# Kernel tuning notes

Hardware: AMD Instinct MI355X
Metric: run time of the kernel (lower is better)

Reference implementation:

```python
import jax, jax.numpy as jnp
import numpy as np

N = 100_000   # nodes
E = 1_600_000 # edges (COO, directed as given)
D = 128       # input feature dim
H = 128       # hidden dim
L = 3         # layers


def setup_inputs() -> dict:
    key = jax.random.key(0)
    ks = jax.random.split(key, 2 + 2 * L)
    x = jax.random.normal(ks[0], (N, D), dtype=jnp.float32)
    edge_index = jax.random.randint(ks[1], (2, E), 0, N, dtype=jnp.int32)
    inp = {"x": x, "edge_index": edge_index}
    dims = [(D, H), (H, H), (H, H)]
    for i, (fi, fo) in enumerate(dims):
        scale = 1.0 / np.sqrt(fi)
        inp[f"W{i}"] = jax.random.uniform(ks[2 + 2 * i], (fi, fo), jnp.float32, -scale, scale)
        inp[f"b{i}"] = jax.random.uniform(ks[3 + 2 * i], (fo,), jnp.float32, -scale, scale)
    return inp


def reference(x, edge_index, W0, b0, W1, b1, W2, b2):
    n = x.shape[0]
    src, dst = edge_index[0], edge_index[1]
    # GCNConv default: add self-loops, symmetric D^{-1/2}(A+I)D^{-1/2} normalization
    loop = jnp.arange(n, dtype=edge_index.dtype)
    src = jnp.concatenate([src, loop])
    dst = jnp.concatenate([dst, loop])
    ones = jnp.ones(src.shape[0], dtype=x.dtype)
    deg = jax.ops.segment_sum(ones, dst, num_segments=n)          # [N]
    dinv = jnp.where(deg > 0, jax.lax.rsqrt(deg), 0.0)            # deg^{-1/2}, inf->0
    norm = dinv[src] * dinv[dst]                                  # [E+N]

    def gcn_conv(h, W, b):
        h = h @ W                                  # linear transform first (PyG order)
        msg = h[src] * norm[:, None]               # gather + scale, [E+N, H]
        return jax.ops.segment_sum(msg, dst, num_segments=n) + b

    for W, b in ((W0, b0), (W1, b1), (W2, b2)):
        x = jax.nn.relu(gcn_conv(x, W, b))
    return x
```

## Files before the change

### kernel.cpp

```cpp
#include <hip/hip_runtime.h>
#include <hip/hip_bf16.h>

#define TPB 256

typedef short s8v __attribute__((ext_vector_type(8)));
typedef float f4v __attribute__((ext_vector_type(4)));
typedef _Float16 h8v __attribute__((ext_vector_type(8)));

#define PB 128
#define BSHIFT 10
#define BSPAN 1024
#define PCHUNK 4096

__device__ __forceinline__ unsigned short bf16_rne(float v) {
    unsigned int u = __float_as_uint(v);
    u += 0x7fffu + ((u >> 16) & 1u);
    return (unsigned short)(u >> 16);
}
__device__ __forceinline__ void split_bf16(float v, unsigned short& hi, unsigned short& lo) {
    hi = bf16_rne(v);
    float hf = __uint_as_float((unsigned int)hi << 16);
    lo = bf16_rne(v - hf);
}


__global__ __launch_bounds__(256) void bhist_kernel(const int* __restrict__ dst, int E,
                                                    int* __restrict__ bsize) {
    __shared__ int h[PB];
    int t = threadIdx.x;
    if (t < PB) h[t] = 0;
    __syncthreads();
    for (int e = blockIdx.x * 256 + t; e < E; e += gridDim.x * 256)
        atomicAdd(&h[dst[e] >> BSHIFT], 1);
    __syncthreads();
    if (t < PB && h[t] > 0) atomicAdd(&bsize[t], h[t]);
}

__global__ void bscan_kernel(const int* __restrict__ bsize, int* __restrict__ bbase,
                             int* __restrict__ bcursor, int* __restrict__ row, int n, int E) {
    __shared__ int wtot[2];
    int t = threadIdx.x;
    int sz = bsize[t];
    int lane = t & 63, wid = t >> 6;
    int v = sz;
    for (int off = 1; off < 64; off <<= 1) {
        int u = __shfl_up(v, off);
        if (lane >= off) v += u;
    }
    if (lane == 63) wtot[wid] = v;
    __syncthreads();
    if (wid == 1) v += wtot[0];
    bbase[t + 1] = v;
    bcursor[t] = v - sz;
    if (t == 0) { bbase[0] = 0; row[n] = E; }
}

__global__ __launch_bounds__(256) void partition_kernel(const int* __restrict__ src,
                                                        const int* __restrict__ dst, int E,
                                                        int* __restrict__ bcursor,
                                                        int2* __restrict__ part) {
    __shared__ int h[PB];
    __shared__ int gofs[PB];
    int t = threadIdx.x;
    long base = (long)blockIdx.x * PCHUNK;
    int cnt = (int)min((long)PCHUNK, (long)E - base);

    if (t < PB) h[t] = 0;
    __syncthreads();
    for (int j = t; j < cnt; j += 256)
        atomicAdd(&h[dst[base + j] >> BSHIFT], 1);
    __syncthreads();
    if (t < PB) gofs[t] = (h[t] > 0) ? atomicAdd(&bcursor[t], h[t]) : 0;
    __syncthreads();
    if (t < PB) h[t] = 0;
    __syncthreads();
    for (int j = t; j < cnt; j += 256) {
        int s = src[base + j], d = dst[base + j];
        int b = d >> BSHIFT;
        int idx = atomicAdd(&h[b], 1);
        part[(long)gofs[b] + idx] = make_int2(s, d);
    }
}

__global__ __launch_bounds__(1024) void csr_kernel(const int2* __restrict__ part,
                                                   const int* __restrict__ bbase,
                                                   int* __restrict__ row, float* __restrict__ dinv,
                                                   int* __restrict__ esrc, int n) {
    __shared__ int deg[BSPAN];
    __shared__ int lrow[BSPAN];
    __shared__ int cur[BSPAN];
    __shared__ int wsum[16];
    int b = blockIdx.x;
    int n0 = b << BSHIFT;
    int nn = min(BSPAN, n - n0);
    if (nn <= 0) return;
    int e0 = bbase[b], e1 = bbase[b + 1];
    int t = threadIdx.x;

    deg[t] = 0;
    __syncthreads();
    for (int e = e0 + t; e < e1; e += 1024)
        atomicAdd(&deg[part[e].y - n0], 1);
    __syncthreads();

    int a = deg[t];
    int lane = t & 63, wid = t >> 6;
    int v = a;
    for (int off = 1; off < 64; off <<= 1) {
        int u = __shfl_up(v, off);
        if (lane >= off) v += u;
    }
    if (lane == 63) wsum[wid] = v;
    __syncthreads();
    if (wid == 0 && lane < 16) {
        int w = wsum[lane];
        for (int off = 1; off < 16; off <<= 1) {
            int u = __shfl_up(w, off);
            if (lane >= off) w += u;
        }
        wsum[lane] = w;
    }
    __syncthreads();
    int excl = v - a + ((wid > 0) ? wsum[wid - 1] : 0);
    lrow[t] = excl;
    cur[t] = 0;
    if (t < nn) {
        row[n0 + t] = e0 + excl;
        dinv[n0 + t] = rsqrtf((float)(deg[t] + 1));
    }
    __syncthreads();

    for (int e = e0 + t; e < e1; e += 1024) {
        int2 p = part[e];
        int d = p.y - n0;
        int idx = atomicAdd(&cur[d], 1);
        esrc[e0 + lrow[d] + idx] = p.x;
    }
}


__global__ void wsplit_kernel(const float* __restrict__ W0, const float* __restrict__ W1,
                              const float* __restrict__ W2,
                              unsigned short* __restrict__ Whi, unsigned short* __restrict__ Wlo) {
    int t = blockIdx.x * TPB + threadIdx.x;
    if (t >= 3 * 16384) return;
    int layer = t >> 14;
    int e = t & 16383;
    int k = e >> 7, ncol = e & 127;
    const float* W = (layer == 0) ? W0 : (layer == 1) ? W1 : W2;
    unsigned short hi, lo;
    split_bf16(W[e], hi, lo);
    int ct = ncol >> 4;
    int lane = (((k >> 3) & 3) << 4) | (ncol & 15);
    int kki = k >> 5;
    int j = k & 7;
    int idx = layer * 16384 + (((ct * 4 + kki) * 64 + lane) * 8 + j);
    Whi[idx] = hi; Wlo[idx] = lo;
}


__global__ __launch_bounds__(256, 2) void gemm0_mfma(const float* __restrict__ Xf,
                                                     const unsigned short* __restrict__ Whs,
                                                     const unsigned short* __restrict__ Wls,
                                                     _Float16* __restrict__ Ch, int n) {
    __shared__ _Float16 Oh[128 * 128];
    int t = threadIdx.x;
    int wave = t >> 6, lane = t & 63;
    int ch = wave & 1, rh = wave >> 1;
    int lm = lane & 15, q = lane >> 4;
    long row0 = (long)blockIdx.x * 128 + rh * 64;

    const s8v* Wh8 = (const s8v*)Whs;
    const s8v* Wl8 = (const s8v*)Wls;
    s8v Bh[4][4], Bl[4][4];
#pragma unroll
    for (int ct = 0; ct < 4; ct++)
#pragma unroll
        for (int kki = 0; kki < 4; kki++) {
            int idx = (((ch * 4 + ct) * 4 + kki) * 64) + lane;
            Bh[ct][kki] = Wh8[idx];
            Bl[ct][kki] = Wl8[idx];
        }

    f4v acc[4][4];
#pragma unroll
    for (int rt = 0; rt < 4; rt++)
#pragma unroll
        for (int ct = 0; ct < 4; ct++) acc[rt][ct] = (f4v)0.0f;

#pragma unroll
    for (int kki = 0; kki < 4; kki++) {
        s8v ah[4], al[4];
#pragma unroll
        for (int rt = 0; rt < 4; rt++) {
            long r = row0 + rt * 16 + lm;
            long rr = (r < n) ? r : (n - 1);
            const float4* xf4 = (const float4*)(Xf + rr * 128 + kki * 32 + q * 8);
            float4 u0 = xf4[0], u1 = xf4[1];
            float uf[8] = {u0.x, u0.y, u0.z, u0.w, u1.x, u1.y, u1.z, u1.w};
            s8v hv, lv;
#pragma unroll
            for (int j = 0; j < 8; j++) {
                unsigned short hh, ll;
                split_bf16(uf[j], hh, ll);
                hv[j] = (short)hh; lv[j] = (short)ll;
            }
            ah[rt] = hv; al[rt] = lv;
        }
#pragma unroll
        for (int rt = 0; rt < 4; rt++)
#pragma unroll
            for (int ct = 0; ct < 4; ct++) {
                acc[rt][ct] = __builtin_amdgcn_mfma_f32_16x16x32_bf16(ah[rt], Bh[ct][kki], acc[rt][ct], 0, 0, 0);
                acc[rt][ct] = __builtin_amdgcn_mfma_f32_16x16x32_bf16(ah[rt], Bl[ct][kki], acc[rt][ct], 0, 0, 0);
                acc[rt][ct] = __builtin_amdgcn_mfma_f32_16x16x32_bf16(al[rt], Bh[ct][kki], acc[rt][ct], 0, 0, 0);
            }
    }

#pragma unroll
    for (int rt = 0; rt < 4; rt++)
#pragma unroll
        for (int reg = 0; reg < 4; reg++) {
            int lr = rh * 64 + rt * 16 + q * 4 + reg;
#pragma unroll
            for (int ct = 0; ct < 4; ct++)
                Oh[lr * 128 + ch * 64 + ct * 16 + lm] = (_Float16)acc[rt][ct][reg];
        }
    __syncthreads();

    long rowb = (long)blockIdx.x * 128;
    int lr = t >> 1;
    int cb = (t & 1) * 64;
    if (rowb + lr < n) {
        const uint4* s = (const uint4*)&Oh[lr * 128 + cb];
        uint4* d = (uint4*)&Ch[(rowb + lr) * 128 + cb];
#pragma unroll
        for (int u = 0; u < 8; u++) d[u] = s[u];
    }
}


__global__ __launch_bounds__(256) void fused_kernel(const h8v* __restrict__ hIn,
                                                    const float* __restrict__ dinv,
                                                    const int* __restrict__ row,
                                                    const int* __restrict__ esrc,
                                                    const float* __restrict__ bias,
                                                    const unsigned short* __restrict__ Whs,
                                                    const unsigned short* __restrict__ Wls,
                                                    _Float16* __restrict__ hOut, int n) {
    __shared__ float As[16 * 132];
    int t = threadIdx.x;
    int g = t >> 4, lane = t & 15;
    long i = (long)blockIdx.x * 16 + g;

    float r[8];
    if (i < n) {
        float di = dinv[i];
        float s2 = di * di;
        h8v self = hIn[i * 16 + lane];
        float acc[8];
#pragma unroll
        for (int k = 0; k < 8; k++) acc[k] = (float)self[k] * s2;

        int e0 = row[i], e1 = row[i + 1];
        int e = e0;
        for (; e + 4 <= e1; e += 4) {
            int s0 = esrc[e + 0];
            int s1 = esrc[e + 1];
            int s2i = esrc[e + 2];
            int s3 = esrc[e + 3];
            h8v v0 = hIn[(size_t)s0 * 16 + lane];
            h8v v1 = hIn[(size_t)s1 * 16 + lane];
            h8v v2 = hIn[(size_t)s2i * 16 + lane];
            h8v v3 = hIn[(size_t)s3 * 16 + lane];
            float w0 = dinv[s0] * di;
            float w1 = dinv[s1] * di;
            float w2 = dinv[s2i] * di;
            float w3 = dinv[s3] * di;
#pragma unroll
            for (int k = 0; k < 8; k++)
                acc[k] += w0 * (float)v0[k] + w1 * (float)v1[k] + w2 * (float)v2[k] + w3 * (float)v3[k];
        }
        for (; e < e1; ++e) {
            int s = esrc[e];
            h8v v = hIn[(size_t)s * 16 + lane];
            float w = dinv[s] * di;
#pragma unroll
            for (int k = 0; k < 8; k++) acc[k] += w * (float)v[k];
        }

        const float4* b4 = (const float4*)(bias + lane * 8);
        float4 bA = b4[0], bB = b4[1];
        r[0] = fmaxf(acc[0] + bA.x, 0.f); r[1] = fmaxf(acc[1] + bA.y, 0.f);
        r[2] = fmaxf(acc[2] + bA.z, 0.f); r[3] = fmaxf(acc[3] + bA.w, 0.f);
        r[4] = fmaxf(acc[4] + bB.x, 0.f); r[5] = fmaxf(acc[5] + bB.y, 0.f);
        r[6] = fmaxf(acc[6] + bB.z, 0.f); r[7] = fmaxf(acc[7] + bB.w, 0.f);
    } else {
#pragma unroll
        for (int k = 0; k < 8; k++) r[k] = 0.f;
    }

    float* dstA = &As[g * 132 + lane * 8];
    *(float4*)dstA = make_float4(r[0], r[1], r[2], r[3]);
    *(float4*)(dstA + 4) = make_float4(r[4], r[5], r[6], r[7]);
    __syncthreads();

    int w = t >> 6, l64 = t & 63;
    int lm = l64 & 15, q = l64 >> 4;

    const s8v* Wh8 = (const s8v*)Whs;
    const s8v* Wl8 = (const s8v*)Wls;
    s8v Bh[2][4], Bl[2][4];
#pragma unroll
    for (int c = 0; c < 2; c++)
#pragma unroll
        for (int kki = 0; kki < 4; kki++) {
            int idx = (((w * 2 + c) * 4 + kki) * 64) + l64;
            Bh[c][kki] = Wh8[idx];
            Bl[c][kki] = Wl8[idx];
        }

    f4v acc2[2];
    acc2[0] = (f4v)0.0f; acc2[1] = (f4v)0.0f;

#pragma unroll
    for (int kki = 0; kki < 4; kki++) {
        const float* ap = &As[lm * 132 + kki * 32 + q * 8];
        float4 u0 = *(const float4*)ap;
        float4 u1 = *(const float4*)(ap + 4);
        float uf[8] = {u0.x, u0.y, u0.z, u0.w, u1.x, u1.y, u1.z, u1.w};
        s8v hv, lv;
#pragma unroll
        for (int j = 0; j < 8; j++) {
            unsigned short hh, ll;
            split_bf16(uf[j], hh, ll);
            hv[j] = (short)hh; lv[j] = (short)ll;
        }
#pragma unroll
        for (int c = 0; c < 2; c++) {
            acc2[c] = __builtin_amdgcn_mfma_f32_16x16x32_bf16(hv, Bh[c][kki], acc2[c], 0, 0, 0);
            acc2[c] = __builtin_amdgcn_mfma_f32_16x16x32_bf16(hv, Bl[c][kki], acc2[c], 0, 0, 0);
            acc2[c] = __builtin_amdgcn_mfma_f32_16x16x32_bf16(lv, Bh[c][kki], acc2[c], 0, 0, 0);
        }
    }
    __syncthreads();

    _Float16* Oh = (_Float16*)As;
#pragma unroll
    for (int c = 0; c < 2; c++)
#pragma unroll
        for (int reg = 0; reg < 4; reg++)
            Oh[(q * 4 + reg) * 128 + (w * 2 + c) * 16 + lm] = (_Float16)acc2[c][reg];
    __syncthreads();

    long gi = (long)blockIdx.x * 16 + (t >> 4);
    if (gi < n) {
        uint4 v = *(const uint4*)&Oh[t * 8];
        *(uint4*)&hOut[gi * 128 + (size_t)(t & 15) * 8] = v;
    }
}


__global__ __launch_bounds__(256) void agg_final(const h8v* __restrict__ hH,
                                                 const float* __restrict__ dinv,
                                                 const int* __restrict__ row,
                                                 const int* __restrict__ esrc,
                                                 const float* __restrict__ bias,
                                                 float* __restrict__ out, int n) {
    int g    = threadIdx.x >> 4;
    int lane = threadIdx.x & 15;
    int i = blockIdx.x * 16 + g;
    if (i >= n) return;

    float di = dinv[i];
    float s2 = di * di;

    h8v self = hH[(size_t)i * 16 + lane];
    float acc[8];
#pragma unroll
    for (int k = 0; k < 8; k++) acc[k] = (float)self[k] * s2;

    int e0 = row[i], e1 = row[i + 1];
    int e = e0;
    for (; e + 4 <= e1; e += 4) {
        int s0 = esrc[e + 0];
        int s1 = esrc[e + 1];
        int s2i = esrc[e + 2];
        int s3 = esrc[e + 3];
        h8v v0 = hH[(size_t)s0 * 16 + lane];
        h8v v1 = hH[(size_t)s1 * 16 + lane];
        h8v v2 = hH[(size_t)s2i * 16 + lane];
        h8v v3 = hH[(size_t)s3 * 16 + lane];
        float w0 = dinv[s0] * di;
        float w1 = dinv[s1] * di;
        float w2 = dinv[s2i] * di;
        float w3 = dinv[s3] * di;
#pragma unroll
        for (int k = 0; k < 8; k++)
            acc[k] += w0 * (float)v0[k] + w1 * (float)v1[k] + w2 * (float)v2[k] + w3 * (float)v3[k];
    }
    for (; e < e1; ++e) {
        int s = esrc[e];
        h8v v = hH[(size_t)s * 16 + lane];
        float w = dinv[s] * di;
#pragma unroll
        for (int k = 0; k < 8; k++) acc[k] += w * (float)v[k];
    }

    const float4* b4 = (const float4*)(bias + lane * 8);
    float4 bA = b4[0], bB = b4[1];
    float4* o4 = (float4*)(out + (size_t)i * 128 + lane * 8);
    o4[0] = make_float4(fmaxf(acc[0] + bA.x, 0.f), fmaxf(acc[1] + bA.y, 0.f),
                        fmaxf(acc[2] + bA.z, 0.f), fmaxf(acc[3] + bA.w, 0.f));
    o4[1] = make_float4(fmaxf(acc[4] + bB.x, 0.f), fmaxf(acc[5] + bB.y, 0.f),
                        fmaxf(acc[6] + bB.z, 0.f), fmaxf(acc[7] + bB.w, 0.f));
}


extern "C" void kernel_launch(void* const* d_in, const int* in_sizes, int n_in,
                              void* d_out, int out_size, void* d_ws, size_t ws_size,
                              hipStream_t stream) {
    const float* x  = (const float*)d_in[0];
    const int*   ei = (const int*)d_in[1];
    const float* W0 = (const float*)d_in[2];
    const float* b0 = (const float*)d_in[3];
    const float* W1 = (const float*)d_in[4];
    const float* b1 = (const float*)d_in[5];
    const float* W2 = (const float*)d_in[6];
    const float* b2 = (const float*)d_in[7];

    const int H = 128;
    int n = in_sizes[0] / H;
    int E = in_sizes[1] / 2;
    const int* srcp = ei;
    const int* dstp = ei + E;

    int gemm_blocks = (n + 127) / 128;
    long npad = (long)gemm_blocks * 128;
    int nbuck = (n + BSPAN - 1) >> BSHIFT;

    char* p = (char*)d_ws;
    auto alloc = [&](size_t bytes) {
        void* r = (void*)p;
        p += (bytes + 255) & ~(size_t)255;
        return r;
    };
    _Float16* bufH0 = (_Float16*)alloc((size_t)npad * H * 2);
    _Float16* bufH1 = (_Float16*)alloc((size_t)npad * H * 2);
    unsigned short* Whs = (unsigned short*)alloc(3 * 16384 * 2);
    unsigned short* Wls = (unsigned short*)alloc(3 * 16384 * 2);
    float* dinv  = (float*)alloc((size_t)n * sizeof(float));
    int*  row    = (int*)alloc((size_t)(n + 1) * sizeof(int));
    int*  bsize  = (int*)alloc(PB * sizeof(int));
    int*  bbase  = (int*)alloc((PB + 1) * sizeof(int));
    int*  bcursor= (int*)alloc(PB * sizeof(int));
    int2* part   = (int2*)alloc((size_t)E * sizeof(int2));
    int*  esrc   = (int*)alloc((size_t)E * sizeof(int));

    hipMemsetAsync(bsize, 0, PB * sizeof(int), stream);

    bhist_kernel<<<1024, 256, 0, stream>>>(dstp, E, bsize);
    bscan_kernel<<<1, PB, 0, stream>>>(bsize, bbase, bcursor, row, n, E);
    partition_kernel<<<(E + PCHUNK - 1) / PCHUNK, 256, 0, stream>>>(srcp, dstp, E, bcursor, part);
    csr_kernel<<<nbuck, 1024, 0, stream>>>(part, bbase, row, dinv, esrc, n);

    wsplit_kernel<<<(3 * 16384 + TPB - 1) / TPB, TPB, 0, stream>>>(W0, W1, W2, Whs, Wls);

    float* out = (float*)d_out;
    int node_blocks = (n + 15) / 16;

    gemm0_mfma<<<gemm_blocks, 256, 0, stream>>>(x, Whs, Wls, bufH0, n);
    fused_kernel<<<node_blocks, 256, 0, stream>>>((const h8v*)bufH0, dinv, row, esrc, b0,
                                                  Whs + 16384, Wls + 16384, bufH1, n);
    fused_kernel<<<node_blocks, 256, 0, stream>>>((const h8v*)bufH1, dinv, row, esrc, b1,
                                                  Whs + 32768, Wls + 32768, bufH0, n);
    agg_final<<<node_blocks, 256, 0, stream>>>((const h8v*)bufH0, dinv, row, esrc, b2, out, n);
}
```

Before: 409.5 us.

## Fuse weight split into histogram kernel, pad LDS tiles, lower gemm0 register use

The weight bf16 hi/lo split now runs in extra blocks of the edge-histogram kernel, which removes one kernel launch. gemm0 loads its B fragments once per k-step instead of holding all of them in registers, and its launch bound asks for 3 blocks per CU to raise occupancy. The LDS output staging tiles in gemm0 and the fused kernel use a row stride of 136 halfs to reduce bank conflicts. The trade-off is that gemm0 reloads its weight fragments from global memory on every k-step and its LDS footprint grows slightly.

```diff
diff --git a/kernel.cpp b/kernel.cpp
--- a/kernel.cpp
+++ b/kernel.cpp
@@ -11,6 +11,7 @@
 #define BSHIFT 10
 #define BSPAN 1024
 #define PCHUNK 4096
+#define WBLK 192
 
 __device__ __forceinline__ unsigned short bf16_rne(float v) {
     unsigned int u = __float_as_uint(v);
@@ -24,13 +25,38 @@
 }
 
 
-__global__ __launch_bounds__(256) void bhist_kernel(const int* __restrict__ dst, int E,
-                                                    int* __restrict__ bsize) {
+__global__ __launch_bounds__(256) void bhist_wsplit_kernel(const int* __restrict__ dst, int E,
+                                                           int* __restrict__ bsize,
+                                                           const float* __restrict__ W0,
+                                                           const float* __restrict__ W1,
+                                                           const float* __restrict__ W2,
+                                                           unsigned short* __restrict__ Whi,
+                                                           unsigned short* __restrict__ Wlo) {
     __shared__ int h[PB];
     int t = threadIdx.x;
+    if (blockIdx.x < WBLK) {
+        int idx0 = blockIdx.x * 256 + t;
+        if (idx0 < 3 * 16384) {
+            int layer = idx0 >> 14;
+            int e = idx0 & 16383;
+            int k = e >> 7, ncol = e & 127;
+            const float* W = (layer == 0) ? W0 : (layer == 1) ? W1 : W2;
+            unsigned short hi, lo;
+            split_bf16(W[e], hi, lo);
+            int ct = ncol >> 4;
+            int lane = (((k >> 3) & 3) << 4) | (ncol & 15);
+            int kki = k >> 5;
+            int j = k & 7;
+            int oidx = layer * 16384 + (((ct * 4 + kki) * 64 + lane) * 8 + j);
+            Whi[oidx] = hi; Wlo[oidx] = lo;
+        }
+        return;
+    }
+    int blk = blockIdx.x - WBLK;
+    int nblk = gridDim.x - WBLK;
     if (t < PB) h[t] = 0;
     __syncthreads();
-    for (int e = blockIdx.x * 256 + t; e < E; e += gridDim.x * 256)
+    for (int e = blk * 256 + t; e < E; e += nblk * 256)
         atomicAdd(&h[dst[e] >> BSHIFT], 1);
     __syncthreads();
     if (t < PB && h[t] > 0) atomicAdd(&bsize[t], h[t]);
@@ -139,31 +165,11 @@
 }
 
 
-__global__ void wsplit_kernel(const float* __restrict__ W0, const float* __restrict__ W1,
-                              const float* __restrict__ W2,
-                              unsigned short* __restrict__ Whi, unsigned short* __restrict__ Wlo) {
-    int t = blockIdx.x * TPB + threadIdx.x;
-    if (t >= 3 * 16384) return;
-    int layer = t >> 14;
-    int e = t & 16383;
-    int k = e >> 7, ncol = e & 127;
-    const float* W = (layer == 0) ? W0 : (layer == 1) ? W1 : W2;
-    unsigned short hi, lo;
-    split_bf16(W[e], hi, lo);
-    int ct = ncol >> 4;
-    int lane = (((k >> 3) & 3) << 4) | (ncol & 15);
-    int kki = k >> 5;
-    int j = k & 7;
-    int idx = layer * 16384 + (((ct * 4 + kki) * 64 + lane) * 8 + j);
-    Whi[idx] = hi; Wlo[idx] = lo;
-}
-
-
-__global__ __launch_bounds__(256, 2) void gemm0_mfma(const float* __restrict__ Xf,
+__global__ __launch_bounds__(256, 3) void gemm0_mfma(const float* __restrict__ Xf,
                                                      const unsigned short* __restrict__ Whs,
                                                      const unsigned short* __restrict__ Wls,
                                                      _Float16* __restrict__ Ch, int n) {
-    __shared__ _Float16 Oh[128 * 128];
+    __shared__ _Float16 Oh[128 * 136];
     int t = threadIdx.x;
     int wave = t >> 6, lane = t & 63;
     int ch = wave & 1, rh = wave >> 1;
@@ -172,24 +178,22 @@
 
     const s8v* Wh8 = (const s8v*)Whs;
     const s8v* Wl8 = (const s8v*)Wls;
-    s8v Bh[4][4], Bl[4][4];
-#pragma unroll
-    for (int ct = 0; ct < 4; ct++)
-#pragma unroll
-        for (int kki = 0; kki < 4; kki++) {
+
+    f4v acc[4][4];
+#pragma unroll
+    for (int rt = 0; rt < 4; rt++)
+#pragma unroll
+        for (int ct = 0; ct < 4; ct++) acc[rt][ct] = (f4v)0.0f;
+
+#pragma unroll
+    for (int kki = 0; kki < 4; kki++) {
+        s8v bh[4], bl[4];
+#pragma unroll
+        for (int ct = 0; ct < 4; ct++) {
             int idx = (((ch * 4 + ct) * 4 + kki) * 64) + lane;
-            Bh[ct][kki] = Wh8[idx];
-            Bl[ct][kki] = Wl8[idx];
-        }
-
-    f4v acc[4][4];
-#pragma unroll
-    for (int rt = 0; rt < 4; rt++)
-#pragma unroll
-        for (int ct = 0; ct < 4; ct++) acc[rt][ct] = (f4v)0.0f;
-
-#pragma unroll
-    for (int kki = 0; kki < 4; kki++) {
+            bh[ct] = Wh8[idx];
+            bl[ct] = Wl8[idx];
+        }
         s8v ah[4], al[4];
 #pragma unroll
         for (int rt = 0; rt < 4; rt++) {
@@ -211,9 +215,9 @@
         for (int rt = 0; rt < 4; rt++)
 #pragma unroll
             for (int ct = 0; ct < 4; ct++) {
-                acc[rt][ct] = __builtin_amdgcn_mfma_f32_16x16x32_bf16(ah[rt], Bh[ct][kki], acc[rt][ct], 0, 0, 0);
-                acc[rt][ct] = __builtin_amdgcn_mfma_f32_16x16x32_bf16(ah[rt], Bl[ct][kki], acc[rt][ct], 0, 0, 0);
-                acc[rt][ct] = __builtin_amdgcn_mfma_f32_16x16x32_bf16(al[rt], Bh[ct][kki], acc[rt][ct], 0, 0, 0);
+                acc[rt][ct] = __builtin_amdgcn_mfma_f32_16x16x32_bf16(ah[rt], bh[ct], acc[rt][ct], 0, 0, 0);
+                acc[rt][ct] = __builtin_amdgcn_mfma_f32_16x16x32_bf16(ah[rt], bl[ct], acc[rt][ct], 0, 0, 0);
+                acc[rt][ct] = __builtin_amdgcn_mfma_f32_16x16x32_bf16(al[rt], bh[ct], acc[rt][ct], 0, 0, 0);
             }
     }
 
@@ -224,7 +228,7 @@
             int lr = rh * 64 + rt * 16 + q * 4 + reg;
 #pragma unroll
             for (int ct = 0; ct < 4; ct++)
-                Oh[lr * 128 + ch * 64 + ct * 16 + lm] = (_Float16)acc[rt][ct][reg];
+                Oh[lr * 136 + ch * 64 + ct * 16 + lm] = (_Float16)acc[rt][ct][reg];
         }
     __syncthreads();
 
@@ -232,7 +236,7 @@
     int lr = t >> 1;
     int cb = (t & 1) * 64;
     if (rowb + lr < n) {
-        const uint4* s = (const uint4*)&Oh[lr * 128 + cb];
+        const uint4* s = (const uint4*)&Oh[lr * 136 + cb];
         uint4* d = (uint4*)&Ch[(rowb + lr) * 128 + cb];
 #pragma unroll
         for (int u = 0; u < 8; u++) d[u] = s[u];
@@ -350,12 +354,12 @@
     for (int c = 0; c < 2; c++)
 #pragma unroll
         for (int reg = 0; reg < 4; reg++)
-            Oh[(q * 4 + reg) * 128 + (w * 2 + c) * 16 + lm] = (_Float16)acc2[c][reg];
+            Oh[(q * 4 + reg) * 136 + (w * 2 + c) * 16 + lm] = (_Float16)acc2[c][reg];
     __syncthreads();
 
     long gi = (long)blockIdx.x * 16 + (t >> 4);
     if (gi < n) {
-        uint4 v = *(const uint4*)&Oh[t * 8];
+        uint4 v = *(const uint4*)&Oh[(t >> 4) * 136 + (t & 15) * 8];
         *(uint4*)&hOut[gi * 128 + (size_t)(t & 15) * 8] = v;
     }
 }
@@ -459,12 +463,10 @@
 
     hipMemsetAsync(bsize, 0, PB * sizeof(int), stream);
 
-    bhist_kernel<<<1024, 256, 0, stream>>>(dstp, E, bsize);
+    bhist_wsplit_kernel<<<WBLK + 1024, 256, 0, stream>>>(dstp, E, bsize, W0, W1, W2, Whs, Wls);
     bscan_kernel<<<1, PB, 0, stream>>>(bsize, bbase, bcursor, row, n, E);
     partition_kernel<<<(E + PCHUNK - 1) / PCHUNK, 256, 0, stream>>>(srcp, dstp, E, bcursor, part);
     csr_kernel<<<nbuck, 1024, 0, stream>>>(part, bbase, row, dinv, esrc, n);
-
-    wsplit_kernel<<<(3 * 16384 + TPB - 1) / TPB, TPB, 0, stream>>>(W0, W1, W2, Whs, Wls);
 
     float* out = (float*)d_out;
     int node_blocks = (n + 15) / 16;
```

After: 404.2 us. Within noise of the previous version (-1.3%).
